# Kernel optimization log

Hardware: AMD Instinct MI355X
Metric: run time of the kernel (lower is better)

Reference implementation:

```python
import jax, jax.numpy as jnp
import numpy as np

B, S, HID = 2, 2048, 1024
NH, HD = 4, 256
SCALE = HD ** -0.5


def _rope(x, fr, fi):
    # x: [B,S,NH,HD]; fr/fi: [S,HD//2]
    b, s, n, d = x.shape
    xr = x.reshape(b, s, n, d // 2, 2)
    re, im = xr[..., 0], xr[..., 1]
    fr = fr[None, :, None, :]
    fi = fi[None, :, None, :]
    rr = re * fr - im * fi
    ri = re * fi + im * fr
    return jnp.stack((rr, ri), axis=-1).reshape(b, s, n, d)


def setup_inputs() -> dict:
    key = jax.random.key(0)
    k1, k2, k3 = jax.random.split(key, 3)
    hidden_states = jax.random.normal(k1, (B, S, HID), dtype=jnp.float32)
    # RoPE frequencies (standard theta=10000)
    inv_freq = 1.0 / (10000.0 ** (np.arange(0, HD, 2, dtype=np.float32) / HD))  # [HD//2]
    t = np.arange(S, dtype=np.float32)
    ang = np.outer(t, inv_freq)  # [S, HD//2]
    freqs_real = jnp.asarray(np.cos(ang), dtype=jnp.float32)
    freqs_imag = jnp.asarray(np.sin(ang), dtype=jnp.float32)
    # causal additive mask [1,1,S,S]
    causal = jnp.tril(jnp.ones((S, S), dtype=bool))
    mask = jnp.where(causal, 0.0, -1e9).astype(jnp.float32)[None, None]
    W_qkv = jax.random.normal(k2, (3 * HID, HID), dtype=jnp.float32) * (HID ** -0.5)
    W_o = jax.random.normal(k3, (HID, HID), dtype=jnp.float32) * (HID ** -0.5)
    return {"hidden_states": hidden_states, "freqs_real": freqs_real,
            "freqs_imag": freqs_imag, "mask": mask, "W_qkv": W_qkv, "W_o": W_o}


def reference(hidden_states, freqs_real, freqs_imag, mask, W_qkv, W_o):
    b, s, _ = hidden_states.shape
    qkv = hidden_states @ W_qkv.T  # [B,S,3*HID]
    qkv = qkv.reshape(b, s, 3, NH, HD)
    q, k, v = qkv[:, :, 0], qkv[:, :, 1], qkv[:, :, 2]
    q = _rope(q, freqs_real, freqs_imag)
    k = _rope(k, freqs_real, freqs_imag)
    scores = jnp.einsum('bqhd,bkhd->bhqk', q * SCALE, k) + mask  # [B,NH,S,S]
    probs = jax.nn.softmax(scores, axis=-1)
    attn = jnp.einsum('bhqk,bkhd->bqhd', probs, v).reshape(b, s, HID)
    return attn @ W_o.T
```

## Files before the change

kernel.cpp:

```cpp
#include <hip/hip_runtime.h>
#include <stdint.h>

#define NB 2
#define NS 2048
#define NHID 1024
#define NHEADS 4
#define DHEAD 256
#define NP 128
#define QK_SCALE 0.0625f

typedef unsigned short ushort_t;
typedef __bf16 bf16x8 __attribute__((ext_vector_type(8)));
typedef float floatx4 __attribute__((ext_vector_type(4)));
typedef short shortx8 __attribute__((ext_vector_type(8)));
typedef unsigned short ushortx4 __attribute__((ext_vector_type(4)));
typedef unsigned short ushortx8 __attribute__((ext_vector_type(8)));

__device__ __forceinline__ float bf2f(ushort_t u) {
    unsigned int x = ((unsigned int)u) << 16;
    return __builtin_bit_cast(float, x);
}
__device__ __forceinline__ ushort_t f2bf(float f) {
    unsigned int u = __builtin_bit_cast(unsigned int, f);
    u += 0x7fff + ((u >> 16) & 1);
    return (ushort_t)(u >> 16);
}

__device__ __forceinline__ floatx4 mfma16(bf16x8 a, bf16x8 b, floatx4 c) {
    return __builtin_amdgcn_mfma_f32_16x16x32_bf16(a, b, c, 0, 0, 0);
}

__device__ __forceinline__ void gload_lds16(const void* g, void* l) {
    __builtin_amdgcn_global_load_lds(
        (const __attribute__((address_space(1))) void*)g,
        (__attribute__((address_space(3))) void*)l, 16, 0, 0);
}

#define N4_H (4096 * 1024 / 4)
#define N4_WQ (3072 * 1024 / 4)
#define N4_WO (1024 * 1024 / 4)
__global__ __launch_bounds__(256) void cast3_kernel(const float* __restrict__ inH,
                                                    const float* __restrict__ inWq,
                                                    const float* __restrict__ inWo,
                                                    ushort_t* __restrict__ out) {
    int i = blockIdx.x * 256 + threadIdx.x;
    const float* src;
    int j = i;
    if (i < N4_H) {
        src = inH;
    } else if (i < N4_H + N4_WQ) {
        src = inWq; j = i - N4_H;
    } else {
        src = inWo; j = i - (N4_H + N4_WQ);
    }
    float4 v = ((const float4*)src)[j];
    ushortx4 o = { f2bf(v.x), f2bf(v.y), f2bf(v.z), f2bf(v.w) };
    ((ushortx4*)out)[i] = o;
}

__global__ __launch_bounds__(256) void gemm_bt_f32(const ushort_t* __restrict__ A,
                                                   const ushort_t* __restrict__ Bt,
                                                   float* __restrict__ Cout,
                                                   int M, int N, int K) {
    __shared__ ushort_t sA[128 * 32];
    __shared__ ushort_t sB[128 * 32];
    const int t = threadIdx.x;
    const int m0 = blockIdx.y * 128;
    const int n0 = blockIdx.x * 128;
    const int w = t >> 6, l = t & 63;
    const int wm = (w >> 1) * 64, wn = (w & 1) * 64;
    const int lc = l & 15, lq = l >> 4;

    floatx4 acc[4][4];
#pragma unroll
    for (int i = 0; i < 4; i++)
#pragma unroll
        for (int j = 0; j < 4; j++) acc[i][j] = (floatx4){0.f, 0.f, 0.f, 0.f};

    const int r0 = t >> 2, c8 = (t & 3) * 8;
    const ushort_t* Ag0 = A + (size_t)(m0 + r0) * K + c8;
    const ushort_t* Ag1 = A + (size_t)(m0 + r0 + 64) * K + c8;
    const ushort_t* Bg0 = Bt + (size_t)(n0 + r0) * K + c8;
    const ushort_t* Bg1 = Bt + (size_t)(n0 + r0 + 64) * K + c8;
    ushort_t* lA0 = &sA[(size_t)t * 8];
    ushort_t* lA1 = &sA[(size_t)(t + 256) * 8];
    ushort_t* lB0 = &sB[(size_t)t * 8];
    ushort_t* lB1 = &sB[(size_t)(t + 256) * 8];

    for (int kk = 0; kk < K; kk += 32) {
        __syncthreads();
        gload_lds16(Ag0 + kk, lA0);
        gload_lds16(Ag1 + kk, lA1);
        gload_lds16(Bg0 + kk, lB0);
        gload_lds16(Bg1 + kk, lB1);
        __syncthreads();
        bf16x8 af[4], bfv[4];
#pragma unroll
        for (int i = 0; i < 4; i++)
            af[i] = *(const bf16x8*)&sA[(wm + i * 16 + lc) * 32 + lq * 8];
#pragma unroll
        for (int j = 0; j < 4; j++)
            bfv[j] = *(const bf16x8*)&sB[(wn + j * 16 + lc) * 32 + lq * 8];
#pragma unroll
        for (int i = 0; i < 4; i++)
#pragma unroll
            for (int j = 0; j < 4; j++)
                acc[i][j] = mfma16(af[i], bfv[j], acc[i][j]);
    }

#pragma unroll
    for (int i = 0; i < 4; i++) {
        int row = m0 + wm + i * 16 + lq * 4;
#pragma unroll
        for (int j = 0; j < 4; j++) {
            int col = n0 + wn + j * 16 + lc;
#pragma unroll
            for (int r = 0; r < 4; r++)
                Cout[(size_t)(row + r) * N + col] = acc[i][j][r];
        }
    }
}

__global__ __launch_bounds__(256) void gemm_qkv(const ushort_t* __restrict__ A,
                                                const ushort_t* __restrict__ Bt,
                                                const float* __restrict__ fre,
                                                const float* __restrict__ fim,
                                                ushort_t* __restrict__ Q,
                                                ushort_t* __restrict__ Kk,
                                                ushort_t* __restrict__ Vt) {
    const int M_K = 1024;
    __shared__ ushort_t sA[128 * 32];
    __shared__ ushort_t sB[128 * 32];
    const int t = threadIdx.x;
    const int m0 = blockIdx.y * 128;
    const int n0 = blockIdx.x * 128;
    const int w = t >> 6, l = t & 63;
    const int wm = (w >> 1) * 64, wn = (w & 1) * 64;
    const int lc = l & 15, lq = l >> 4;

    floatx4 acc[4][4];
#pragma unroll
    for (int i = 0; i < 4; i++)
#pragma unroll
        for (int j = 0; j < 4; j++) acc[i][j] = (floatx4){0.f, 0.f, 0.f, 0.f};

    const int r0 = t >> 2, c8 = (t & 3) * 8;
    const ushort_t* Ag0 = A + (size_t)(m0 + r0) * M_K + c8;
    const ushort_t* Ag1 = A + (size_t)(m0 + r0 + 64) * M_K + c8;
    const ushort_t* Bg0 = Bt + (size_t)(n0 + r0) * M_K + c8;
    const ushort_t* Bg1 = Bt + (size_t)(n0 + r0 + 64) * M_K + c8;
    ushort_t* lA0 = &sA[(size_t)t * 8];
    ushort_t* lA1 = &sA[(size_t)(t + 256) * 8];
    ushort_t* lB0 = &sB[(size_t)t * 8];
    ushort_t* lB1 = &sB[(size_t)(t + 256) * 8];

    for (int kk = 0; kk < M_K; kk += 32) {
        __syncthreads();
        gload_lds16(Ag0 + kk, lA0);
        gload_lds16(Ag1 + kk, lA1);
        gload_lds16(Bg0 + kk, lB0);
        gload_lds16(Bg1 + kk, lB1);
        __syncthreads();
        bf16x8 af[4], bfv[4];
#pragma unroll
        for (int i = 0; i < 4; i++)
            af[i] = *(const bf16x8*)&sA[(wm + i * 16 + lc) * 32 + lq * 8];
#pragma unroll
        for (int j = 0; j < 4; j++)
            bfv[j] = *(const bf16x8*)&sB[(wn + j * 16 + lc) * 32 + lq * 8];
#pragma unroll
        for (int i = 0; i < 4; i++)
#pragma unroll
            for (int j = 0; j < 4; j++)
                acc[i][j] = mfma16(af[i], bfv[j], acc[i][j]);
    }

    const int sect = n0 >> 10;
#pragma unroll
    for (int i = 0; i < 4; i++) {
        int row = m0 + wm + i * 16 + lq * 4;
        int b = row >> 11;
        int srow = row & 2047;
#pragma unroll
        for (int j = 0; j < 4; j++) {
            int col = n0 + wn + j * 16 + lc;
            int d = col & 255;
            int h = (col >> 8) & 3;
            int bh = b * NHEADS + h;
            if (sect == 2) {
                ushortx4 pack = { f2bf(acc[i][j][0]), f2bf(acc[i][j][1]),
                                  f2bf(acc[i][j][2]), f2bf(acc[i][j][3]) };
                *(ushortx4*)&Vt[((size_t)bh * 256 + d) * NS + srow] = pack;
            } else {
                int p = d >> 1;
                int odd = d & 1;
                ushort_t* dst = (sect == 0) ? Q : Kk;
#pragma unroll
                for (int r = 0; r < 4; r++) {
                    float v = acc[i][j][r];
                    float vp = __shfl_xor(v, 1);
                    int s = srow + r;
                    float c = fre[s * NP + p], si = fim[s * NP + p];
                    float out = odd ? (vp * si + v * c) : (v * c - vp * si);
                    if (sect == 0) out *= QK_SCALE;
                    dst[((size_t)bh * NS + s) * DHEAD + d] = f2bf(out);
                }
            }
        }
    }
}

#define BQ3 128
#define BKV3 64
#define PPAD 72
#define NPART_BH 51
#define OPART_SPLIT 224

__global__ __launch_bounds__(256, 2) void flash_attn4(const ushort_t* __restrict__ Q,
                                                      const ushort_t* __restrict__ K,
                                                      const ushort_t* __restrict__ Vt,
                                                      ushort_t* __restrict__ OpA,
                                                      ushort_t* __restrict__ OpB,
                                                      float* __restrict__ ml) {
    __shared__ ushort_t sK[BKV3 * 256];
    __shared__ ushort_t sV[DHEAD * 64];
    __shared__ ushort_t sP[4][16 * PPAD];

    int rem = blockIdx.x, qt = 15, nsp;
    for (;;) {
        nsp = (2 * (qt + 1) + 5) / 6;
        if (rem < nsp) break;
        rem -= nsp;
        qt--;
    }
    const int nch = 2 * (qt + 1);
    const int cbeg = rem * 6;
    const int cend = (cbeg + 6 < nch) ? cbeg + 6 : nch;

    const int h = blockIdx.y, b = blockIdx.z;
    const int t = threadIdx.x, w = t >> 6, l = t & 63;
    const int lc = l & 15, lq = l >> 4;
    const int bh = b * NHEADS + h;
    const size_t base = (size_t)bh * NS * DHEAD;
    const int q0 = qt * BQ3;

    const int krb = w * 2 + (l >> 5);
    const int kck = ((l & 31) - (krb & 7)) & 31;
    const size_t koff = (size_t)krb * 256 + kck * 8;
    const int vrb = w * 8 + (l >> 3);
    const int vck = ((l & 7) - (vrb & 7)) & 7;
    const size_t voff = (size_t)vrb * NS + vck * 8;
    ushort_t* dK = &sK[w * 512 + l * 8];
    ushort_t* dV = &sV[w * 512 + l * 8];

    bf16x8 qf[2][8];
#pragma unroll
    for (int gq = 0; gq < 2; gq++) {
        const ushort_t* qrow = Q + base + (size_t)(q0 + w * 32 + gq * 16 + lc) * DHEAD + lq * 8;
#pragma unroll
        for (int dk = 0; dk < 8; dk++) qf[gq][dk] = *(const bf16x8*)(qrow + dk * 32);
    }

    floatx4 accO[2][16];
#pragma unroll
    for (int gq = 0; gq < 2; gq++)
#pragma unroll
        for (int j = 0; j < 16; j++) accO[gq][j] = (floatx4){0.f, 0.f, 0.f, 0.f};
    float lrun[2][4] = {{0.f, 0.f, 0.f, 0.f}, {0.f, 0.f, 0.f, 0.f}};

    for (int kc = cbeg; kc < cend; kc++) {
        const int kb = kc * BKV3;
        __syncthreads();
        {
            const ushort_t* ksrc = K + base + (size_t)kb * 256 + koff;
            const ushort_t* vsrc = Vt + base + kb + voff;
#pragma unroll
            for (int j = 0; j < 8; j++)
                gload_lds16(ksrc + j * (8 * 256), dK + j * 2048);
#pragma unroll
            for (int j = 0; j < 8; j++)
                gload_lds16(vsrc + j * (32 * NS), dV + j * 2048);
        }
        __syncthreads();

        floatx4 sfr[2][4];
#pragma unroll
        for (int gq = 0; gq < 2; gq++)
#pragma unroll
            for (int g = 0; g < 4; g++) sfr[gq][g] = (floatx4){0.f, 0.f, 0.f, 0.f};
#pragma unroll
        for (int dk = 0; dk < 8; dk++) {
#pragma unroll
            for (int g = 0; g < 4; g++) {
                int R = g * 16 + lc;
                int phys = (dk * 4 + lq + (R & 7)) & 31;
                bf16x8 bk = *(const bf16x8*)&sK[R * 256 + phys * 8];
                sfr[0][g] = mfma16(qf[0][dk], bk, sfr[0][g]);
                sfr[1][g] = mfma16(qf[1][dk], bk, sfr[1][g]);
            }
        }

        if (kc >= nch - 2) {
#pragma unroll
            for (int gq = 0; gq < 2; gq++)
#pragma unroll
                for (int g = 0; g < 4; g++) {
                    int kg = kb + g * 16 + lc;
                    int qr = q0 + w * 32 + gq * 16 + lq * 4;
#pragma unroll
                    for (int r = 0; r < 4; r++)
                        if (kg > qr + r) sfr[gq][g][r] = -1e30f;
                }
        }

        ushort_t* pw = sP[w];
#pragma unroll
        for (int gq = 0; gq < 2; gq++) {
#pragma unroll
            for (int g = 0; g < 4; g++)
#pragma unroll
                for (int r = 0; r < 4; r++) {
                    float p = __expf(sfr[gq][g][r]);
                    lrun[gq][r] += p;
                    pw[(lq * 4 + r) * PPAD + g * 16 + lc] = f2bf(p);
                }
            bf16x8 ap0 = *(const bf16x8*)&pw[lc * PPAD + lq * 8];
            bf16x8 ap1 = *(const bf16x8*)&pw[lc * PPAD + 32 + lq * 8];
#pragma unroll
            for (int j = 0; j < 16; j++) {
                int D = j * 16 + lc;
                int ph0 = (lq + (D & 7)) & 7;
                int ph1 = (4 + lq + (D & 7)) & 7;
                bf16x8 bv0 = *(const bf16x8*)&sV[D * 64 + ph0 * 8];
                bf16x8 bv1 = *(const bf16x8*)&sV[D * 64 + ph1 * 8];
                accO[gq][j] = mfma16(ap0, bv0, accO[gq][j]);
                accO[gq][j] = mfma16(ap1, bv1, accO[gq][j]);
            }
        }
    }

    const int pid = bh * NPART_BH + blockIdx.x;
    ushort_t* op = (pid < OPART_SPLIT) ? OpA + (size_t)pid * (128 * 256)
                                       : OpB + (size_t)(pid - OPART_SPLIT) * (128 * 256);
#pragma unroll
    for (int gq = 0; gq < 2; gq++) {
#pragma unroll
        for (int r = 0; r < 4; r++) {
            int row = w * 32 + gq * 16 + lq * 4 + r;
#pragma unroll
            for (int j = 0; j < 16; j++)
                op[row * 256 + j * 16 + lc] = f2bf(accO[gq][j][r]);
            float lv = lrun[gq][r];
#pragma unroll
            for (int off = 1; off < 16; off <<= 1) lv += __shfl_xor(lv, off);
            if (lc == 0) ml[(size_t)pid * 128 + row] = lv;
        }
    }
}

__global__ __launch_bounds__(256) void combine_parts2(const ushort_t* __restrict__ OpA,
                                                      const ushort_t* __restrict__ OpB,
                                                      const float* __restrict__ ml,
                                                      ushort_t* __restrict__ O) {
    const int qt = blockIdx.x >> 3, rsub = blockIdx.x & 7;
    const int h = blockIdx.y, b = blockIdx.z;
    const int bh = b * NHEADS + h;
    int bbase = 0;
    for (int q = 15; q > qt; q--) bbase += (2 * (q + 1) + 5) / 6;
    const int nsp = (2 * (qt + 1) + 5) / 6;
    const int pid0 = bh * NPART_BH + bbase;

    const int t = threadIdx.x;
    const int rl = t >> 4;
    const int c0 = (t & 15) * 16;
    const int row = rsub * 16 + rl;

    float so[16];
#pragma unroll
    for (int k = 0; k < 16; k++) so[k] = 0.f;
    float sl = 0.f;

    for (int i = 0; i < nsp; i++) {
        int pid = pid0 + i;
        const ushort_t* op = (pid < OPART_SPLIT)
                                 ? OpA + (size_t)pid * (128 * 256)
                                 : OpB + (size_t)(pid - OPART_SPLIT) * (128 * 256);
        const ushort_t* p = op + row * 256 + c0;
        ushortx8 a0 = *(const ushortx8*)p;
        ushortx8 a1 = *(const ushortx8*)(p + 8);
#pragma unroll
        for (int k = 0; k < 8; k++) {
            so[k] += bf2f(a0[k]);
            so[8 + k] += bf2f(a1[k]);
        }
        sl += ml[(size_t)pid * 128 + row];
    }

    float inv = 1.f / sl;
    ushortx8 o0, o1;
#pragma unroll
    for (int k = 0; k < 8; k++) {
        o0[k] = f2bf(so[k] * inv);
        o1[k] = f2bf(so[8 + k] * inv);
    }
    int s = qt * BQ3 + row;
    ushort_t* dst = O + ((size_t)(b * NS + s) * NHEADS + h) * DHEAD + c0;
    *(ushortx8*)dst = o0;
    *(ushortx8*)(dst + 8) = o1;
}

extern "C" void kernel_launch(void* const* d_in, const int* in_sizes, int n_in,
                              void* d_out, int out_size, void* d_ws, size_t ws_size,
                              hipStream_t stream) {
    const float* hidden = (const float*)d_in[0];
    const float* fre = (const float*)d_in[1];
    const float* fim = (const float*)d_in[2];
    const float* Wqkv = (const float*)d_in[4];
    const float* Wo = (const float*)d_in[5];

    char* ws = (char*)d_ws;
    ushort_t* hb    = (ushort_t*)(ws);
    ushort_t* wqkvb = (ushort_t*)(ws + 8388608);
    ushort_t* wob   = (ushort_t*)(ws + 14680064);
    ushort_t* qb    = (ushort_t*)(ws + 16777216);
    ushort_t* kb    = (ushort_t*)(ws + 25165824);
    ushort_t* vtb   = (ushort_t*)(ws + 33554432);
    ushort_t* OpA   = (ushort_t*)(ws);
    ushort_t* OpB   = (ushort_t*)(ws + 41943040);
    float*    ml    = (float*)(ws + 54001664);
    ushort_t* oattn = (ushort_t*)(ws + 16777216);

    cast3_kernel<<<(N4_H + N4_WQ + N4_WO) / 256, 256, 0, stream>>>(hidden, Wqkv, Wo, hb);

    gemm_qkv<<<dim3(3072 / 128, 4096 / 128), 256, 0, stream>>>(
        hb, wqkvb, fre, fim, qb, kb, vtb);

    flash_attn4<<<dim3(NPART_BH, NHEADS, NB), 256, 0, stream>>>(qb, kb, vtb, OpA, OpB, ml);
    combine_parts2<<<dim3(128, NHEADS, NB), 256, 0, stream>>>(OpA, OpB, ml, oattn);

    gemm_bt_f32<<<dim3(1024 / 128, 4096 / 128), 256, 0, stream>>>(
        oattn, wob, (float*)d_out, 4096, 1024, 1024);
}
```

Before: 224.1 us.

## Use BK=64 swizzled LDS tiles in GEMMs and split-K the output projection

Both GEMMs now stage 64-wide K tiles in LDS with an XOR-style swizzle, which halves the number of barrier pairs per K and is meant to avoid LDS bank conflicts. The output projection is split into two K halves across blockIdx.z, doubling its 256-block grid to 512 for better occupancy. The two fp32 partial results go to workspace and are summed by an extra elementwise add kernel. This adds one kernel launch and about 48MB of extra fp32 traffic. The ml buffer is moved to a new workspace offset, and the chunk-size macro CHCAP is only a rename.

```diff
diff --git a/kernel.cpp b/kernel.cpp
--- a/kernel.cpp
+++ b/kernel.cpp
@@ -58,15 +58,20 @@
     ((ushortx4*)out)[i] = o;
 }
 
-__global__ __launch_bounds__(256) void gemm_bt_f32(const ushort_t* __restrict__ A,
-                                                   const ushort_t* __restrict__ Bt,
-                                                   float* __restrict__ Cout,
-                                                   int M, int N, int K) {
-    __shared__ ushort_t sA[128 * 32];
-    __shared__ ushort_t sB[128 * 32];
+
+__global__ __launch_bounds__(256) void gemm_bt_f32s(const ushort_t* __restrict__ A,
+                                                    const ushort_t* __restrict__ Bt,
+                                                    float* __restrict__ C0,
+                                                    float* __restrict__ C1,
+                                                    int M, int N, int K) {
+    __shared__ ushort_t sA[128 * 64];
+    __shared__ ushort_t sB[128 * 64];
     const int t = threadIdx.x;
     const int m0 = blockIdx.y * 128;
     const int n0 = blockIdx.x * 128;
+    const int kz = blockIdx.z;
+    float* Cout = kz ? C1 : C0;
+    const int kbeg = kz * (K / 2), kend = kbeg + K / 2;
     const int w = t >> 6, l = t & 63;
     const int wm = (w >> 1) * 64, wn = (w & 1) * 64;
     const int lc = l & 15, lq = l >> 4;
@@ -77,35 +82,40 @@
 #pragma unroll
         for (int j = 0; j < 4; j++) acc[i][j] = (floatx4){0.f, 0.f, 0.f, 0.f};
 
-    const int r0 = t >> 2, c8 = (t & 3) * 8;
-    const ushort_t* Ag0 = A + (size_t)(m0 + r0) * K + c8;
-    const ushort_t* Ag1 = A + (size_t)(m0 + r0 + 64) * K + c8;
-    const ushort_t* Bg0 = Bt + (size_t)(n0 + r0) * K + c8;
-    const ushort_t* Bg1 = Bt + (size_t)(n0 + r0 + 64) * K + c8;
-    ushort_t* lA0 = &sA[(size_t)t * 8];
-    ushort_t* lA1 = &sA[(size_t)(t + 256) * 8];
-    ushort_t* lB0 = &sB[(size_t)t * 8];
-    ushort_t* lB1 = &sB[(size_t)(t + 256) * 8];
-
-    for (int kk = 0; kk < K; kk += 32) {
-        __syncthreads();
-        gload_lds16(Ag0 + kk, lA0);
-        gload_lds16(Ag1 + kk, lA1);
-        gload_lds16(Bg0 + kk, lB0);
-        gload_lds16(Bg1 + kk, lB1);
-        __syncthreads();
-        bf16x8 af[4], bfv[4];
-#pragma unroll
-        for (int i = 0; i < 4; i++)
-            af[i] = *(const bf16x8*)&sA[(wm + i * 16 + lc) * 32 + lq * 8];
-#pragma unroll
-        for (int j = 0; j < 4; j++)
-            bfv[j] = *(const bf16x8*)&sB[(wn + j * 16 + lc) * 32 + lq * 8];
-#pragma unroll
-        for (int i = 0; i < 4; i++)
-#pragma unroll
-            for (int j = 0; j < 4; j++)
-                acc[i][j] = mfma16(af[i], bfv[j], acc[i][j]);
+    const int srow = w * 8 + (l >> 3);
+    const int scol = ((((l & 7) - (l >> 3)) & 7)) * 8;
+    const ushort_t* Ag = A + (size_t)(m0 + srow) * K + scol;
+    const ushort_t* Bg = Bt + (size_t)(n0 + srow) * K + scol;
+    ushort_t* lA = &sA[(size_t)t * 8];
+    ushort_t* lB = &sB[(size_t)t * 8];
+
+    for (int kk = kbeg; kk < kend; kk += 64) {
+        __syncthreads();
+#pragma unroll
+        for (int j = 0; j < 4; j++) {
+            gload_lds16(Ag + kk + (size_t)j * 32 * K, lA + j * 2048);
+            gload_lds16(Bg + kk + (size_t)j * 32 * K, lB + j * 2048);
+        }
+        __syncthreads();
+#pragma unroll
+        for (int ks = 0; ks < 2; ks++) {
+            bf16x8 af[4], bfv[4];
+#pragma unroll
+            for (int i = 0; i < 4; i++) {
+                int R = wm + i * 16 + lc;
+                af[i] = *(const bf16x8*)&sA[R * 64 + ((ks * 4 + lq + R) & 7) * 8];
+            }
+#pragma unroll
+            for (int j = 0; j < 4; j++) {
+                int R = wn + j * 16 + lc;
+                bfv[j] = *(const bf16x8*)&sB[R * 64 + ((ks * 4 + lq + R) & 7) * 8];
+            }
+#pragma unroll
+            for (int i = 0; i < 4; i++)
+#pragma unroll
+                for (int j = 0; j < 4; j++)
+                    acc[i][j] = mfma16(af[i], bfv[j], acc[i][j]);
+        }
     }
 
 #pragma unroll
@@ -118,6 +128,18 @@
             for (int r = 0; r < 4; r++)
                 Cout[(size_t)(row + r) * N + col] = acc[i][j][r];
         }
+    }
+}
+
+__global__ __launch_bounds__(256) void add_f32(const float* __restrict__ a,
+                                               const float* __restrict__ b,
+                                               float* __restrict__ o, int n4) {
+    int i = blockIdx.x * 256 + threadIdx.x;
+    if (i < n4) {
+        float4 x = ((const float4*)a)[i];
+        float4 y = ((const float4*)b)[i];
+        float4 z = { x.x + y.x, x.y + y.y, x.z + y.z, x.w + y.w };
+        ((float4*)o)[i] = z;
     }
 }
 
@@ -129,8 +151,8 @@
                                                 ushort_t* __restrict__ Kk,
                                                 ushort_t* __restrict__ Vt) {
     const int M_K = 1024;
-    __shared__ ushort_t sA[128 * 32];
-    __shared__ ushort_t sB[128 * 32];
+    __shared__ ushort_t sA[128 * 64];
+    __shared__ ushort_t sB[128 * 64];
     const int t = threadIdx.x;
     const int m0 = blockIdx.y * 128;
     const int n0 = blockIdx.x * 128;
@@ -144,35 +166,40 @@
 #pragma unroll
         for (int j = 0; j < 4; j++) acc[i][j] = (floatx4){0.f, 0.f, 0.f, 0.f};
 
-    const int r0 = t >> 2, c8 = (t & 3) * 8;
-    const ushort_t* Ag0 = A + (size_t)(m0 + r0) * M_K + c8;
-    const ushort_t* Ag1 = A + (size_t)(m0 + r0 + 64) * M_K + c8;
-    const ushort_t* Bg0 = Bt + (size_t)(n0 + r0) * M_K + c8;
-    const ushort_t* Bg1 = Bt + (size_t)(n0 + r0 + 64) * M_K + c8;
-    ushort_t* lA0 = &sA[(size_t)t * 8];
-    ushort_t* lA1 = &sA[(size_t)(t + 256) * 8];
-    ushort_t* lB0 = &sB[(size_t)t * 8];
-    ushort_t* lB1 = &sB[(size_t)(t + 256) * 8];
-
-    for (int kk = 0; kk < M_K; kk += 32) {
-        __syncthreads();
-        gload_lds16(Ag0 + kk, lA0);
-        gload_lds16(Ag1 + kk, lA1);
-        gload_lds16(Bg0 + kk, lB0);
-        gload_lds16(Bg1 + kk, lB1);
-        __syncthreads();
-        bf16x8 af[4], bfv[4];
-#pragma unroll
-        for (int i = 0; i < 4; i++)
-            af[i] = *(const bf16x8*)&sA[(wm + i * 16 + lc) * 32 + lq * 8];
-#pragma unroll
-        for (int j = 0; j < 4; j++)
-            bfv[j] = *(const bf16x8*)&sB[(wn + j * 16 + lc) * 32 + lq * 8];
-#pragma unroll
-        for (int i = 0; i < 4; i++)
-#pragma unroll
-            for (int j = 0; j < 4; j++)
-                acc[i][j] = mfma16(af[i], bfv[j], acc[i][j]);
+    const int srow = w * 8 + (l >> 3);
+    const int scol = ((((l & 7) - (l >> 3)) & 7)) * 8;
+    const ushort_t* Ag = A + (size_t)(m0 + srow) * M_K + scol;
+    const ushort_t* Bg = Bt + (size_t)(n0 + srow) * M_K + scol;
+    ushort_t* lA = &sA[(size_t)t * 8];
+    ushort_t* lB = &sB[(size_t)t * 8];
+
+    for (int kk = 0; kk < M_K; kk += 64) {
+        __syncthreads();
+#pragma unroll
+        for (int j = 0; j < 4; j++) {
+            gload_lds16(Ag + kk + (size_t)j * 32 * M_K, lA + j * 2048);
+            gload_lds16(Bg + kk + (size_t)j * 32 * M_K, lB + j * 2048);
+        }
+        __syncthreads();
+#pragma unroll
+        for (int ks = 0; ks < 2; ks++) {
+            bf16x8 af[4], bfv[4];
+#pragma unroll
+            for (int i = 0; i < 4; i++) {
+                int R = wm + i * 16 + lc;
+                af[i] = *(const bf16x8*)&sA[R * 64 + ((ks * 4 + lq + R) & 7) * 8];
+            }
+#pragma unroll
+            for (int j = 0; j < 4; j++) {
+                int R = wn + j * 16 + lc;
+                bfv[j] = *(const bf16x8*)&sB[R * 64 + ((ks * 4 + lq + R) & 7) * 8];
+            }
+#pragma unroll
+            for (int i = 0; i < 4; i++)
+#pragma unroll
+                for (int j = 0; j < 4; j++)
+                    acc[i][j] = mfma16(af[i], bfv[j], acc[i][j]);
+        }
     }
 
     const int sect = n0 >> 10;
@@ -180,7 +207,7 @@
     for (int i = 0; i < 4; i++) {
         int row = m0 + wm + i * 16 + lq * 4;
         int b = row >> 11;
-        int srow = row & 2047;
+        int srow2 = row & 2047;
 #pragma unroll
         for (int j = 0; j < 4; j++) {
             int col = n0 + wn + j * 16 + lc;
@@ -190,7 +217,7 @@
             if (sect == 2) {
                 ushortx4 pack = { f2bf(acc[i][j][0]), f2bf(acc[i][j][1]),
                                   f2bf(acc[i][j][2]), f2bf(acc[i][j][3]) };
-                *(ushortx4*)&Vt[((size_t)bh * 256 + d) * NS + srow] = pack;
+                *(ushortx4*)&Vt[((size_t)bh * 256 + d) * NS + srow2] = pack;
             } else {
                 int p = d >> 1;
                 int odd = d & 1;
@@ -199,7 +226,7 @@
                 for (int r = 0; r < 4; r++) {
                     float v = acc[i][j][r];
                     float vp = __shfl_xor(v, 1);
-                    int s = srow + r;
+                    int s = srow2 + r;
                     float c = fre[s * NP + p], si = fim[s * NP + p];
                     float out = odd ? (vp * si + v * c) : (v * c - vp * si);
                     if (sect == 0) out *= QK_SCALE;
@@ -213,6 +240,7 @@
 #define BQ3 128
 #define BKV3 64
 #define PPAD 72
+#define CHCAP 6
 #define NPART_BH 51
 #define OPART_SPLIT 224
 
@@ -228,14 +256,14 @@
 
     int rem = blockIdx.x, qt = 15, nsp;
     for (;;) {
-        nsp = (2 * (qt + 1) + 5) / 6;
+        nsp = (2 * (qt + 1) + CHCAP - 1) / CHCAP;
         if (rem < nsp) break;
         rem -= nsp;
         qt--;
     }
     const int nch = 2 * (qt + 1);
-    const int cbeg = rem * 6;
-    const int cend = (cbeg + 6 < nch) ? cbeg + 6 : nch;
+    const int cbeg = rem * CHCAP;
+    const int cend = (cbeg + CHCAP < nch) ? cbeg + CHCAP : nch;
 
     const int h = blockIdx.y, b = blockIdx.z;
     const int t = threadIdx.x, w = t >> 6, l = t & 63;
@@ -366,8 +394,8 @@
     const int h = blockIdx.y, b = blockIdx.z;
     const int bh = b * NHEADS + h;
     int bbase = 0;
-    for (int q = 15; q > qt; q--) bbase += (2 * (q + 1) + 5) / 6;
-    const int nsp = (2 * (qt + 1) + 5) / 6;
+    for (int q = 15; q > qt; q--) bbase += (2 * (q + 1) + CHCAP - 1) / CHCAP;
+    const int nsp = (2 * (qt + 1) + CHCAP - 1) / CHCAP;
     const int pid0 = bh * NPART_BH + bbase;
 
     const int t = threadIdx.x;
@@ -427,8 +455,10 @@
     ushort_t* vtb   = (ushort_t*)(ws + 33554432);
     ushort_t* OpA   = (ushort_t*)(ws);
     ushort_t* OpB   = (ushort_t*)(ws + 41943040);
-    float*    ml    = (float*)(ws + 54001664);
     ushort_t* oattn = (ushort_t*)(ws + 16777216);
+    float*    gP0   = (float*)(ws + 25165824);
+    float*    gP1   = (float*)(ws + 41943040);
+    float*    ml    = (float*)(ws + 58720256);
 
     cast3_kernel<<<(N4_H + N4_WQ + N4_WO) / 256, 256, 0, stream>>>(hidden, Wqkv, Wo, hb);
 
@@ -438,6 +468,7 @@
     flash_attn4<<<dim3(NPART_BH, NHEADS, NB), 256, 0, stream>>>(qb, kb, vtb, OpA, OpB, ml);
     combine_parts2<<<dim3(128, NHEADS, NB), 256, 0, stream>>>(OpA, OpB, ml, oattn);
 
-    gemm_bt_f32<<<dim3(1024 / 128, 4096 / 128), 256, 0, stream>>>(
-        oattn, wob, (float*)d_out, 4096, 1024, 1024);
-}
+    gemm_bt_f32s<<<dim3(1024 / 128, 4096 / 128, 2), 256, 0, stream>>>(
+        oattn, wob, gP0, gP1, 4096, 1024, 1024);
+    add_f32<<<4096, 256, 0, stream>>>(gP0, gP1, (float*)d_out, 4096 * 1024 / 4);
+}
```

New measurement: 208.6 us. 1.07x faster.
